# Optimization experiments

Hardware: AMD Instinct MI355X
Metric: run time of the kernel (lower is better)

The kernel has to match this reference:

```python
import jax, jax.numpy as jnp
import numpy as np

H, W = 64, 64
C = 256
NH = 8
WS = 8
SS = 4
N = WS * WS
HD = C // NH
HIDDEN = 4 * C
CPB_HIDDEN = 512
EPS = 1e-6


def _window_partition(x, ws):
    B, H_, W_, C_ = x.shape
    x = x.reshape(B, H_ // ws, ws, W_ // ws, ws, C_).transpose(0, 1, 3, 2, 4, 5)
    return x.reshape(-1, ws, ws, C_)


def _window_reverse(win, ws, H_, W_):
    B = win.shape[0] // ((H_ // ws) * (W_ // ws))
    x = win.reshape(B, H_ // ws, W_ // ws, ws, ws, -1).transpose(0, 1, 3, 2, 4, 5)
    return x.reshape(B, H_, W_, -1)


def _coords_table():
    # (1, 2*WS-1, 2*WS-1, 2) log-spaced continuous relative coords (SwinV2 CPB)
    ch = np.arange(-(WS - 1), WS)
    cw = np.arange(-(WS - 1), WS)
    t = np.stack(np.meshgrid(ch, cw, indexing='ij'), axis=-1)[None].astype(np.float32)
    t = t / (WS - 1) * 8.0
    t = np.sign(t) * np.log2(np.abs(t) + 1.0) / np.log2(8.0)
    return t.astype(np.float32)


def _rpe_index():
    coords = np.stack(np.meshgrid(np.arange(WS), np.arange(WS), indexing='ij'))
    cf = coords.reshape(2, -1)
    rel = (cf[:, :, None] - cf[:, None, :]).transpose(1, 2, 0)
    rel[:, :, 0] += WS - 1
    rel[:, :, 1] += WS - 1
    rel[:, :, 0] *= 2 * WS - 1
    return rel.sum(-1)  # (N, N) int


def _attn_mask():
    img = np.zeros((1, H, W, 1), np.float32)
    cnt = 0
    for hs in (slice(0, -WS), slice(-WS, -SS), slice(-SS, None)):
        for ws_ in (slice(0, -WS), slice(-WS, -SS), slice(-SS, None)):
            img[:, hs, ws_, :] = cnt
            cnt += 1
    mw = img.reshape(1, H // WS, WS, W // WS, WS, 1).transpose(0, 1, 3, 2, 4, 5).reshape(-1, N)
    am = mw[:, None, :] - mw[:, :, None]
    return np.where(am != 0, -100.0, 0.0).astype(np.float32)  # (nW, N, N)


_TABLE = jnp.asarray(_coords_table())
_RPE = jnp.asarray(_rpe_index().reshape(-1))
_AMASK = jnp.asarray(_attn_mask())


def setup_inputs() -> dict:
    key = jax.random.key(0)
    ks = jax.random.split(key, 12)
    s = 0.02
    return {
        'x': jax.random.normal(ks[0], (32, H * W, C), jnp.float32),
        'qkv_w': jax.random.normal(ks[1], (C, 3 * C), jnp.float32) * s,
        'q_bias': jnp.zeros((C,), jnp.float32),
        'v_bias': jnp.zeros((C,), jnp.float32),
        'logit_scale': jnp.log(10.0 * jnp.ones((NH, 1, 1), jnp.float32)),
        'cpb_w1': jax.random.normal(ks[2], (2, CPB_HIDDEN), jnp.float32) * s,
        'cpb_b1': jnp.zeros((CPB_HIDDEN,), jnp.float32),
        'cpb_w2': jax.random.normal(ks[3], (CPB_HIDDEN, NH), jnp.float32) * s,
        'proj_w': jax.random.normal(ks[4], (C, C), jnp.float32) * s,
        'proj_b': jnp.zeros((C,), jnp.float32),
        'norm1_scale': jnp.ones((C,), jnp.float32),
        'norm1_bias': jnp.zeros((C,), jnp.float32),
        'norm2_scale': jnp.ones((C,), jnp.float32),
        'norm2_bias': jnp.zeros((C,), jnp.float32),
        'fc1_w': jax.random.normal(ks[5], (C, HIDDEN), jnp.float32) * s,
        'fc1_b': jnp.zeros((HIDDEN,), jnp.float32),
        'fc2_w': jax.random.normal(ks[6], (HIDDEN, C), jnp.float32) * s,
        'fc2_b': jnp.zeros((C,), jnp.float32),
    }


def _layernorm(y, scale, bias):
    mu = jnp.mean(y, axis=-1, keepdims=True)
    var = jnp.mean(jnp.square(y - mu), axis=-1, keepdims=True)
    return (y - mu) * jax.lax.rsqrt(var + EPS) * scale + bias


def _l2n(t):
    return t * jax.lax.rsqrt(jnp.maximum(jnp.sum(t * t, axis=-1, keepdims=True), 1e-12))


def reference(x, qkv_w, q_bias, v_bias, logit_scale, cpb_w1, cpb_b1, cpb_w2,
              proj_w, proj_b, norm1_scale, norm1_bias, norm2_scale, norm2_bias,
              fc1_w, fc1_b, fc2_w, fc2_b):
    B, L, C_ = x.shape
    nW = _AMASK.shape[0]
    shortcut = x

    # cyclic shift + window partition
    xi = x.reshape(B, H, W, C_)
    xi = jnp.roll(xi, (-SS, -SS), axis=(1, 2))
    xw = _window_partition(xi, WS).reshape(-1, N, C_)  # (B_, N, C)
    B_ = xw.shape[0]

    # qkv with q/v bias only (k bias is zero)
    qkv_bias = jnp.concatenate([q_bias, jnp.zeros_like(v_bias), v_bias])
    qkv = xw @ qkv_w + qkv_bias
    qkv = qkv.reshape(B_, N, 3, NH, HD).transpose(2, 0, 3, 1, 4)
    q, k, v = qkv[0], qkv[1], qkv[2]  # (B_, NH, N, HD)

    # cosine attention with learned clamped logit scale
    attn = jnp.einsum('bhnd,bhmd->bhnm', _l2n(q), _l2n(k))
    scale = jnp.exp(jnp.minimum(logit_scale, np.log(100.0)))  # (NH,1,1)
    attn = attn * scale

    # continuous-position-bias MLP -> relative position bias, 16*sigmoid
    bias_table = jax.nn.relu(_TABLE @ cpb_w1 + cpb_b1) @ cpb_w2  # (1,2WS-1,2WS-1,NH)
    bias_table = bias_table.reshape(-1, NH)
    rpb = bias_table[_RPE].reshape(N, N, NH).transpose(2, 0, 1)  # (NH,N,N)
    attn = attn + (16.0 * jax.nn.sigmoid(rpb))[None]

    # shifted-window mask
    attn = attn.reshape(B_ // nW, nW, NH, N, N) + _AMASK[None, :, None]
    attn = jax.nn.softmax(attn.reshape(B_, NH, N, N), axis=-1)

    out = jnp.einsum('bhnm,bhmd->bnhd', attn, v).reshape(B_, N, C_)
    out = out @ proj_w + proj_b

    # window reverse + reverse cyclic shift
    out = _window_reverse(out.reshape(-1, WS, WS, C_), WS, H, W)
    out = jnp.roll(out, (SS, SS), axis=(1, 2)).reshape(B, L, C_)

    # SwinV2 post-norm residuals
    x1 = shortcut + _layernorm(out, norm1_scale, norm1_bias)
    h = jax.nn.gelu(x1 @ fc1_w + fc1_b) @ fc2_w + fc2_b
    return x1 + _layernorm(h, norm2_scale, norm2_bias)
```

## Files before the change

### kernel.cpp

```cpp
#include <hip/hip_runtime.h>

typedef __bf16 bf16;
typedef __bf16 bf16x8 __attribute__((ext_vector_type(8)));
typedef __bf16 bf16x4 __attribute__((ext_vector_type(4)));
typedef float  f32x4  __attribute__((ext_vector_type(4)));

#define MFMA16(a, b, c) __builtin_amdgcn_mfma_f32_16x16x32_bf16(a, b, c, 0, 0, 0)

__device__ __forceinline__ void gload_lds16(const void* g, void* l) {
    __builtin_amdgcn_global_load_lds((const __attribute__((address_space(1))) void*)g,
                                     (__attribute__((address_space(3))) void*)l, 16, 0, 0);
}

__device__ __forceinline__ long win2orig(long r) {
    long b = r >> 12; int rem = (int)(r & 4095);
    int widx = rem >> 6, t = rem & 63;
    int rp = ((widx >> 3) << 3) + (t >> 3), cp = ((widx & 7) << 3) + (t & 7);
    int rr = (rp + 4) & 63, cc = (cp + 4) & 63;
    return (b << 12) + rr * 64 + cc;
}

template <int GELU>
__global__ __launch_bounds__(256) void gemm_bt(const bf16* __restrict__ A,
                                               const bf16* __restrict__ Bt,
                                               const float* __restrict__ bias,
                                               bf16* __restrict__ C,
                                               int M, int N, int K) {
    __shared__ bf16 As[2][4096];
    __shared__ bf16 Bs[2][4096];
    const int t = threadIdx.x;
    const int w = t >> 6, l = t & 63;
    const int l15 = l & 15, q4 = l >> 4;
    const int wm = w >> 1, wn = w & 1;

    const unsigned gx = gridDim.x;
    const unsigned nwg = gx * gridDim.y;
    const unsigned id0 = blockIdx.y * gx + blockIdx.x;
    const unsigned swz = (id0 & 7u) * (nwg >> 3) + (id0 >> 3);
    const unsigned bx = swz % gx, by = swz / gx;

    const long row0 = (long)by * 128;
    const int col0 = (int)bx * 128;

    const bf16* aP = A + (row0 + w * 16 + l15) * (long)K + q4 * 8;
    const bf16* bP = Bt + (long)(col0 + w * 16 + l15) * K + q4 * 8;
    const long step64 = 64L * K;

    f32x4 acc[4][4];
#pragma unroll
    for (int i = 0; i < 4; i++)
#pragma unroll
        for (int j = 0; j < 4; j++)
#pragma unroll
            for (int r = 0; r < 4; r++) acc[i][j][r] = 0.f;

    const int KT = K >> 5;

    gload_lds16(aP,          &As[0][w * 512]);
    gload_lds16(aP + step64, &As[0][w * 512 + 2048]);
    gload_lds16(bP,          &Bs[0][w * 512]);
    gload_lds16(bP + step64, &Bs[0][w * 512 + 2048]);
    aP += 32; bP += 32;
    gload_lds16(aP,          &As[1][w * 512]);
    gload_lds16(aP + step64, &As[1][w * 512 + 2048]);
    gload_lds16(bP,          &Bs[1][w * 512]);
    gload_lds16(bP + step64, &Bs[1][w * 512 + 2048]);
    aP += 32; bP += 32;

    for (int kt = 0; kt < KT; ++kt) {
        const int cur = kt & 1;
        if (kt < KT - 1) { asm volatile("s_waitcnt vmcnt(4)" ::: "memory"); }
        else             { asm volatile("s_waitcnt vmcnt(0)" ::: "memory"); }
        __builtin_amdgcn_s_barrier();
        asm volatile("" ::: "memory");

        bf16x8 af[4], bfv[4];
#pragma unroll
        for (int mi = 0; mi < 4; mi++) af[mi] = *(const bf16x8*)(&As[cur][(wm * 4 + mi) * 512 + l * 8]);
#pragma unroll
        for (int nj = 0; nj < 4; nj++) bfv[nj] = *(const bf16x8*)(&Bs[cur][(wn * 4 + nj) * 512 + l * 8]);

        asm volatile("s_waitcnt lgkmcnt(0)" ::: "memory");
        __builtin_amdgcn_sched_barrier(0);
        __builtin_amdgcn_s_barrier();
        asm volatile("" ::: "memory");

        if (kt + 2 < KT) {
            gload_lds16(aP,          &As[cur][w * 512]);
            gload_lds16(aP + step64, &As[cur][w * 512 + 2048]);
            gload_lds16(bP,          &Bs[cur][w * 512]);
            gload_lds16(bP + step64, &Bs[cur][w * 512 + 2048]);
            aP += 32; bP += 32;
        }
        __builtin_amdgcn_sched_barrier(0);

#pragma unroll
        for (int mi = 0; mi < 4; mi++)
#pragma unroll
            for (int nj = 0; nj < 4; nj++) acc[mi][nj] = MFMA16(af[mi], bfv[nj], acc[mi][nj]);
    }

    float cb[4];
#pragma unroll
    for (int nj = 0; nj < 4; nj++) cb[nj] = bias[col0 + wn * 64 + nj * 16 + l15];

#pragma unroll
    for (int mi = 0; mi < 4; mi++) {
#pragma unroll
        for (int reg = 0; reg < 4; reg++) {
            long r = row0 + wm * 64 + mi * 16 + q4 * 4 + reg;
            bf16* cpn = C + r * (long)N + col0 + wn * 64 + l15;
#pragma unroll
            for (int nj = 0; nj < 4; nj++) {
                float v = acc[mi][nj][reg] + cb[nj];
                if (GELU) {
                    float v2 = v * v;
                    float tt = v * fmaf(v2, -0.10294702f, -2.30218094f);
                    float e = __builtin_amdgcn_exp2f(tt);
                    v = v * __builtin_amdgcn_rcpf(1.f + e);
                }
                cpn[nj * 16] = (bf16)v;
            }
        }
    }
}

__global__ __launch_bounds__(64) void attn_kernel(const bf16* __restrict__ qkv,
                                                  const float* __restrict__ bias16,
                                                  const float* __restrict__ logit_scale,
                                                  bf16* __restrict__ outp) {
    __shared__ bf16 P[64 * 72];
    __shared__ bf16 Vt[32 * 72];
    const int unit = blockIdx.x;
    const int w = unit >> 3, h = unit & 7;
    const int l = threadIdx.x;
    const int l15 = l & 15, q4 = l >> 4;
    const bf16* base = qkv + (long)w * 64 * 768;

    {
        const bf16* vp = base + l * 768 + 512 + h * 32;
#pragma unroll
        for (int c = 0; c < 4; c++) {
            bf16x8 vv = *(const bf16x8*)(vp + c * 8);
#pragma unroll
            for (int j = 0; j < 8; j++) Vt[(c * 8 + j) * 72 + l] = vv[j];
        }
    }

    const float scale = __expf(fminf(logit_scale[h], 4.605170186f));

    bf16x8 qf[4], kf[4];
#pragma unroll
    for (int mi = 0; mi < 4; mi++) {
        const bf16* p = base + (mi * 16 + l15) * 768 + h * 32 + q4 * 8;
        bf16x8 xv = *(const bf16x8*)p;
        float fv[8]; float ss = 0.f;
#pragma unroll
        for (int j = 0; j < 8; j++) { fv[j] = (float)xv[j]; ss += fv[j] * fv[j]; }
        ss += __shfl_xor(ss, 16); ss += __shfl_xor(ss, 32);
        float rs = rsqrtf(fmaxf(ss, 1e-12f));
#pragma unroll
        for (int j = 0; j < 8; j++) qf[mi][j] = (bf16)(fv[j] * rs);
    }
#pragma unroll
    for (int nj = 0; nj < 4; nj++) {
        const bf16* p = base + (nj * 16 + l15) * 768 + 256 + h * 32 + q4 * 8;
        bf16x8 xv = *(const bf16x8*)p;
        float fv[8]; float ss = 0.f;
#pragma unroll
        for (int j = 0; j < 8; j++) { fv[j] = (float)xv[j]; ss += fv[j] * fv[j]; }
        ss += __shfl_xor(ss, 16); ss += __shfl_xor(ss, 32);
        float rs = rsqrtf(fmaxf(ss, 1e-12f));
#pragma unroll
        for (int j = 0; j < 8; j++) kf[nj][j] = (bf16)(fv[j] * rs);
    }

    f32x4 acc[4][4];
#pragma unroll
    for (int i = 0; i < 4; i++)
#pragma unroll
        for (int j = 0; j < 4; j++)
#pragma unroll
            for (int r = 0; r < 4; r++) acc[i][j][r] = 0.f;
#pragma unroll
    for (int mi = 0; mi < 4; mi++)
#pragma unroll
        for (int nj = 0; nj < 4; nj++) acc[mi][nj] = MFMA16(qf[mi], kf[nj], acc[mi][nj]);

    const int widx = w & 63, wr = widx >> 3, wc = widx & 7;
    const bool edge = (wr == 7) || (wc == 7);
    int crid[4];
    if (edge) {
#pragma unroll
        for (int nj = 0; nj < 4; nj++) {
            int m = nj * 16 + l15;
            int R = wr * 8 + (m >> 3), Cc = wc * 8 + (m & 7);
            crid[nj] = ((R < 56) ? 0 : (R < 60 ? 1 : 2)) * 3 + ((Cc < 56) ? 0 : (Cc < 60 ? 1 : 2));
        }
    }
    const float* bh = bias16 + h * 4096;
#pragma unroll
    for (int mi = 0; mi < 4; mi++) {
#pragma unroll
        for (int reg = 0; reg < 4; reg++) {
            int n = mi * 16 + q4 * 4 + reg;
            const float* bp = bh + n * 64;
            int nrid = 0;
            if (edge) {
                int R = wr * 8 + (n >> 3), Cc = wc * 8 + (n & 7);
                nrid = ((R < 56) ? 0 : (R < 60 ? 1 : 2)) * 3 + ((Cc < 56) ? 0 : (Cc < 60 ? 1 : 2));
            }
#pragma unroll
            for (int nj = 0; nj < 4; nj++) {
                float v = acc[mi][nj][reg] * scale + bp[nj * 16 + l15];
                if (edge && nrid != crid[nj]) v -= 100.f;
                acc[mi][nj][reg] = v;
            }
        }
    }

#pragma unroll
    for (int mi = 0; mi < 4; mi++) {
#pragma unroll
        for (int reg = 0; reg < 4; reg++) {
            float mx = fmaxf(fmaxf(acc[mi][0][reg], acc[mi][1][reg]),
                             fmaxf(acc[mi][2][reg], acc[mi][3][reg]));
            mx = fmaxf(mx, __shfl_xor(mx, 1));
            mx = fmaxf(mx, __shfl_xor(mx, 2));
            mx = fmaxf(mx, __shfl_xor(mx, 4));
            mx = fmaxf(mx, __shfl_xor(mx, 8));
            float s = 0.f;
#pragma unroll
            for (int nj = 0; nj < 4; nj++) {
                float e = __expf(acc[mi][nj][reg] - mx);
                acc[mi][nj][reg] = e; s += e;
            }
            s += __shfl_xor(s, 1); s += __shfl_xor(s, 2);
            s += __shfl_xor(s, 4); s += __shfl_xor(s, 8);
            float inv = 1.f / s;
            int n = mi * 16 + q4 * 4 + reg;
#pragma unroll
            for (int nj = 0; nj < 4; nj++)
                P[n * 72 + nj * 16 + l15] = (bf16)(acc[mi][nj][reg] * inv);
        }
    }
    __syncthreads();

    f32x4 o[4][2];
#pragma unroll
    for (int i = 0; i < 4; i++)
#pragma unroll
        for (int j = 0; j < 2; j++)
#pragma unroll
            for (int r = 0; r < 4; r++) o[i][j][r] = 0.f;
#pragma unroll
    for (int ks = 0; ks < 2; ks++) {
        bf16x8 vf[2];
#pragma unroll
        for (int nj = 0; nj < 2; nj++) vf[nj] = *(const bf16x8*)(&Vt[(nj * 16 + l15) * 72 + ks * 32 + q4 * 8]);
#pragma unroll
        for (int mi = 0; mi < 4; mi++) {
            bf16x8 pf = *(const bf16x8*)(&P[(mi * 16 + l15) * 72 + ks * 32 + q4 * 8]);
#pragma unroll
            for (int nj = 0; nj < 2; nj++) o[mi][nj] = MFMA16(pf, vf[nj], o[mi][nj]);
        }
    }

    bf16* op = outp + (long)w * 64 * 256 + h * 32;
#pragma unroll
    for (int mi = 0; mi < 4; mi++)
#pragma unroll
        for (int reg = 0; reg < 4; reg++) {
            int tok = mi * 16 + q4 * 4 + reg;
#pragma unroll
            for (int nj = 0; nj < 2; nj++)
                op[tok * 256 + nj * 16 + l15] = (bf16)o[mi][nj][reg];
        }
}

__global__ __launch_bounds__(256) void norm1_kernel(const bf16* __restrict__ pin,
                                                    const float* __restrict__ x,
                                                    const float* __restrict__ g,
                                                    const float* __restrict__ bb,
                                                    bf16* __restrict__ x1h) {
    const int tid = threadIdx.x;
    const int wid = tid >> 6, l = tid & 63;
    const long rl = (long)blockIdx.x * 4 + wid;
    bf16x4 v4 = *(const bf16x4*)(pin + rl * 256 + l * 4);
    float v[4]; float s = 0.f, sq = 0.f;
#pragma unroll
    for (int c = 0; c < 4; c++) { v[c] = (float)v4[c]; s += v[c]; sq += v[c] * v[c]; }
#pragma unroll
    for (int off = 1; off < 64; off <<= 1) { s += __shfl_xor(s, off); sq += __shfl_xor(sq, off); }
    float mu = s * 0.00390625f;
    float var = sq * 0.00390625f - mu * mu;
    float rstd = rsqrtf(var + 1e-6f);
    long orig = win2orig(rl);
    float4 xv = *(const float4*)(x + orig * 256 + l * 4);
    float4 gv = *(const float4*)(g + l * 4);
    float4 bv = *(const float4*)(bb + l * 4);
    bf16x4 oh;
    oh[0] = (bf16)(xv.x + ((v[0] - mu) * rstd * gv.x + bv.x));
    oh[1] = (bf16)(xv.y + ((v[1] - mu) * rstd * gv.y + bv.y));
    oh[2] = (bf16)(xv.z + ((v[2] - mu) * rstd * gv.z + bv.z));
    oh[3] = (bf16)(xv.w + ((v[3] - mu) * rstd * gv.w + bv.w));
    *(bf16x4*)(x1h + orig * 256 + l * 4) = oh;
}

__global__ __launch_bounds__(256) void norm2_kernel(const bf16* __restrict__ hin,
                                                    const bf16* __restrict__ x1h,
                                                    const float* __restrict__ g,
                                                    const float* __restrict__ bb,
                                                    float* __restrict__ outp) {
    const int tid = threadIdx.x;
    const int wid = tid >> 6, l = tid & 63;
    const long rl = (long)blockIdx.x * 4 + wid;
    bf16x4 v4 = *(const bf16x4*)(hin + rl * 256 + l * 4);
    float v[4]; float s = 0.f, sq = 0.f;
#pragma unroll
    for (int c = 0; c < 4; c++) { v[c] = (float)v4[c]; s += v[c]; sq += v[c] * v[c]; }
#pragma unroll
    for (int off = 1; off < 64; off <<= 1) { s += __shfl_xor(s, off); sq += __shfl_xor(sq, off); }
    float mu = s * 0.00390625f;
    float var = sq * 0.00390625f - mu * mu;
    float rstd = rsqrtf(var + 1e-6f);
    bf16x4 xv4 = *(const bf16x4*)(x1h + rl * 256 + l * 4);
    float4 gv = *(const float4*)(g + l * 4);
    float4 bv = *(const float4*)(bb + l * 4);
    float4 ov;
    ov.x = (float)xv4[0] + ((v[0] - mu) * rstd * gv.x + bv.x);
    ov.y = (float)xv4[1] + ((v[1] - mu) * rstd * gv.y + bv.y);
    ov.z = (float)xv4[2] + ((v[2] - mu) * rstd * gv.z + bv.z);
    ov.w = (float)xv4[3] + ((v[3] - mu) * rstd * gv.w + bv.w);
    *(float4*)(outp + rl * 256 + l * 4) = ov;
}

__global__ __launch_bounds__(256) void gather_cast(const float* __restrict__ x,
                                                   bf16* __restrict__ out) {
    const int tid = threadIdx.x;
    const int wid = tid >> 6, l = tid & 63;
    const long rl = (long)blockIdx.x * 4 + wid;
    long orig = win2orig(rl);
    float4 v = *(const float4*)(x + orig * 256 + l * 4);
    bf16x4 o = {(bf16)v.x, (bf16)v.y, (bf16)v.z, (bf16)v.w};
    *(bf16x4*)(out + rl * 256 + l * 4) = o;
}

__global__ void transpose_cast(const float* __restrict__ in, bf16* __restrict__ out, int K, int N) {
    int id = blockIdx.x * 256 + threadIdx.x;
    if (id < K * N) {
        int n = id / K, k = id - n * K;
        out[id] = (bf16)in[k * N + n];
    }
}

__global__ void build_qkv_bias(const float* __restrict__ qb, const float* __restrict__ vb,
                               float* __restrict__ out) {
    int i = blockIdx.x * 256 + threadIdx.x;
    if (i < 768) out[i] = (i < 256) ? qb[i] : ((i < 512) ? 0.f : vb[i - 512]);
}

__device__ __forceinline__ float cpcoord(int d) {
    float v = (float)d * (8.0f / 7.0f);
    float r = log2f(fabsf(v) + 1.0f) * (1.0f / 3.0f);
    return v < 0.f ? -r : r;
}

__global__ void cpb1(const float* __restrict__ w1, const float* __restrict__ b1,
                     const float* __restrict__ w2, float* __restrict__ tbl) {
    int a = threadIdx.x;
    if (a >= 225) return;
    int i = a / 15, j = a - i * 15;
    float t0 = cpcoord(i - 7), t1 = cpcoord(j - 7);
    float acc[8];
#pragma unroll
    for (int o = 0; o < 8; o++) acc[o] = 0.f;
    for (int jj = 0; jj < 512; jj++) {
        float hv = fmaf(t0, w1[jj], fmaf(t1, w1[512 + jj], b1[jj]));
        hv = fmaxf(hv, 0.f);
#pragma unroll
        for (int o = 0; o < 8; o++) acc[o] = fmaf(hv, w2[jj * 8 + o], acc[o]);
    }
#pragma unroll
    for (int o = 0; o < 8; o++) tbl[a * 8 + o] = acc[o];
}

__global__ void cpb2(const float* __restrict__ tbl, float* __restrict__ bias16) {
    int id = blockIdx.x * 256 + threadIdx.x;
    if (id >= 32768) return;
    int h = id >> 12, n = (id >> 6) & 63, m = id & 63;
    int r0 = (n >> 3) - (m >> 3) + 7;
    int r1 = (n & 7) - (m & 7) + 7;
    float v = tbl[(r0 * 15 + r1) * 8 + h];
    bias16[id] = 16.f / (1.f + __expf(-v));
}

extern "C" void kernel_launch(void* const* d_in, const int* in_sizes, int n_in,
                              void* d_out, int out_size, void* d_ws, size_t ws_size,
                              hipStream_t stream) {
    const float* x   = (const float*)d_in[0];
    const float* qkvw= (const float*)d_in[1];
    const float* qb  = (const float*)d_in[2];
    const float* vb  = (const float*)d_in[3];
    const float* ls  = (const float*)d_in[4];
    const float* cw1 = (const float*)d_in[5];
    const float* cb1 = (const float*)d_in[6];
    const float* cw2 = (const float*)d_in[7];
    const float* pw  = (const float*)d_in[8];
    const float* pb  = (const float*)d_in[9];
    const float* n1s = (const float*)d_in[10];
    const float* n1b = (const float*)d_in[11];
    const float* n2s = (const float*)d_in[12];
    const float* n2b = (const float*)d_in[13];
    const float* f1w = (const float*)d_in[14];
    const float* f1b = (const float*)d_in[15];
    const float* f2w = (const float*)d_in[16];
    const float* f2b = (const float*)d_in[17];

    char* ws = (char*)d_ws;
    if (ws_size < 471859200UL) return;
    bf16*  qkvBt   = (bf16*)(ws + 0);
    bf16*  projBt  = (bf16*)(ws + 393216);
    bf16*  fc1Bt   = (bf16*)(ws + 524288);
    bf16*  fc2Bt   = (bf16*)(ws + 1048576);
    float* qkvBias = (float*)(ws + 1572864);
    float* cpbTbl  = (float*)(ws + 1575936);
    float* bias16  = (float*)(ws + 1583360);
    bf16* xbf     = (bf16*)(ws + 2097152);
    bf16* qkvBuf  = (bf16*)(ws + 69206016);
    bf16* attnOut = (bf16*)(ws + 270532608);
    bf16* projOut = (bf16*)(ws + 337641472);
    bf16* x1h     = (bf16*)(ws + 404750336);
    bf16* hBuf    = (bf16*)(ws + 2097152);
    bf16* fc2Out  = (bf16*)(ws + 337641472);

    transpose_cast<<<768, 256, 0, stream>>>(qkvw, qkvBt, 256, 768);
    transpose_cast<<<256, 256, 0, stream>>>(pw, projBt, 256, 256);
    transpose_cast<<<1024, 256, 0, stream>>>(f1w, fc1Bt, 256, 1024);
    transpose_cast<<<1024, 256, 0, stream>>>(f2w, fc2Bt, 1024, 256);
    build_qkv_bias<<<3, 256, 0, stream>>>(qb, vb, qkvBias);
    cpb1<<<1, 256, 0, stream>>>(cw1, cb1, cw2, cpbTbl);
    cpb2<<<128, 256, 0, stream>>>(cpbTbl, bias16);

    gather_cast<<<32768, 256, 0, stream>>>(x, xbf);
    gemm_bt<0><<<dim3(6, 1024), 256, 0, stream>>>(xbf, qkvBt, qkvBias, qkvBuf, 131072, 768, 256);
    attn_kernel<<<16384, 64, 0, stream>>>(qkvBuf, bias16, ls, attnOut);
    gemm_bt<0><<<dim3(2, 1024), 256, 0, stream>>>(attnOut, projBt, pb, projOut, 131072, 256, 256);
    norm1_kernel<<<32768, 256, 0, stream>>>(projOut, x, n1s, n1b, x1h);
    gemm_bt<1><<<dim3(8, 1024), 256, 0, stream>>>(x1h, fc1Bt, f1b, hBuf, 131072, 1024, 256);
    gemm_bt<0><<<dim3(2, 1024), 256, 0, stream>>>(hBuf, fc2Bt, f2b, fc2Out, 131072, 256, 1024);
    norm2_kernel<<<32768, 256, 0, stream>>>(fc2Out, x1h, n2s, n2b, (float*)d_out);
}
```

Measured before the change: 1.030 ms.

## Enlarge GEMM tiles to 256x256 with 512 threads and K-step 64

The shared GEMM kernel moves from 128x128 tiles with 4 waves to 256x256 tiles with 8 waves, each wave computing 128x64. Each K iteration now covers 64 elements, split into two 32-wide halves with separate LDS reads, and all four GEMM launches get matching grids. The goal is more reuse of each loaded tile and fewer global loads and barriers per FLOP. The cost is 128KB of LDS per block and a larger accumulator array, which may lower occupancy. The fixed LDS layout with 256x256 tiles also assumes the 16-row staging per wave lines up with the fragment reads.

```diff
diff --git a/kernel.cpp b/kernel.cpp
--- a/kernel.cpp
+++ b/kernel.cpp
@@ -21,17 +21,17 @@
 }
 
 template <int GELU>
-__global__ __launch_bounds__(256) void gemm_bt(const bf16* __restrict__ A,
-                                               const bf16* __restrict__ Bt,
-                                               const float* __restrict__ bias,
-                                               bf16* __restrict__ C,
-                                               int M, int N, int K) {
-    __shared__ bf16 As[2][4096];
-    __shared__ bf16 Bs[2][4096];
+__global__ __launch_bounds__(512, 2) void gemm_bt(const bf16* __restrict__ A,
+                                                  const bf16* __restrict__ Bt,
+                                                  const float* __restrict__ bias,
+                                                  bf16* __restrict__ C,
+                                                  int M, int N, int K) {
+    __shared__ bf16 As[2][16384];
+    __shared__ bf16 Bs[2][16384];
     const int t = threadIdx.x;
     const int w = t >> 6, l = t & 63;
     const int l15 = l & 15, q4 = l >> 4;
-    const int wm = w >> 1, wn = w & 1;
+    const int wm = w >> 2, wn = w & 3;
 
     const unsigned gx = gridDim.x;
     const unsigned nwg = gx * gridDim.y;
@@ -39,76 +39,98 @@
     const unsigned swz = (id0 & 7u) * (nwg >> 3) + (id0 >> 3);
     const unsigned bx = swz % gx, by = swz / gx;
 
-    const long row0 = (long)by * 128;
-    const int col0 = (int)bx * 128;
-
-    const bf16* aP = A + (row0 + w * 16 + l15) * (long)K + q4 * 8;
-    const bf16* bP = Bt + (long)(col0 + w * 16 + l15) * K + q4 * 8;
-    const long step64 = 64L * K;
-
-    f32x4 acc[4][4];
-#pragma unroll
-    for (int i = 0; i < 4; i++)
+    const long row0 = (long)by * 256;
+    const int col0 = (int)bx * 256;
+
+    const bf16* aSrc0; const bf16* aSrc1; const bf16* aSrc2; const bf16* aSrc3;
+    const bf16* bSrc0; const bf16* bSrc1; const bf16* bSrc2; const bf16* bSrc3;
+    {
+        const long ar = row0 + (w * 2) * 16 + l15;
+        const long br = (long)col0 + (w * 2) * 16 + l15;
+        aSrc0 = A + ar * (long)K + q4 * 8;
+        aSrc1 = A + ar * (long)K + 32 + q4 * 8;
+        aSrc2 = A + (ar + 16) * (long)K + q4 * 8;
+        aSrc3 = A + (ar + 16) * (long)K + 32 + q4 * 8;
+        bSrc0 = Bt + br * (long)K + q4 * 8;
+        bSrc1 = Bt + br * (long)K + 32 + q4 * 8;
+        bSrc2 = Bt + (br + 16) * (long)K + q4 * 8;
+        bSrc3 = Bt + (br + 16) * (long)K + 32 + q4 * 8;
+    }
+
+#define STAGE(buf)                                         \
+    do {                                                   \
+        gload_lds16(aSrc0, &As[buf][w * 2048 + 0 * 512]);  \
+        gload_lds16(aSrc1, &As[buf][w * 2048 + 1 * 512]);  \
+        gload_lds16(aSrc2, &As[buf][w * 2048 + 2 * 512]);  \
+        gload_lds16(aSrc3, &As[buf][w * 2048 + 3 * 512]);  \
+        gload_lds16(bSrc0, &Bs[buf][w * 2048 + 0 * 512]);  \
+        gload_lds16(bSrc1, &Bs[buf][w * 2048 + 1 * 512]);  \
+        gload_lds16(bSrc2, &Bs[buf][w * 2048 + 2 * 512]);  \
+        gload_lds16(bSrc3, &Bs[buf][w * 2048 + 3 * 512]);  \
+        aSrc0 += 64; aSrc1 += 64; aSrc2 += 64; aSrc3 += 64;\
+        bSrc0 += 64; bSrc1 += 64; bSrc2 += 64; bSrc3 += 64;\
+    } while (0)
+
+    f32x4 acc[8][4];
+#pragma unroll
+    for (int i = 0; i < 8; i++)
 #pragma unroll
         for (int j = 0; j < 4; j++)
 #pragma unroll
             for (int r = 0; r < 4; r++) acc[i][j][r] = 0.f;
 
-    const int KT = K >> 5;
-
-    gload_lds16(aP,          &As[0][w * 512]);
-    gload_lds16(aP + step64, &As[0][w * 512 + 2048]);
-    gload_lds16(bP,          &Bs[0][w * 512]);
-    gload_lds16(bP + step64, &Bs[0][w * 512 + 2048]);
-    aP += 32; bP += 32;
-    gload_lds16(aP,          &As[1][w * 512]);
-    gload_lds16(aP + step64, &As[1][w * 512 + 2048]);
-    gload_lds16(bP,          &Bs[1][w * 512]);
-    gload_lds16(bP + step64, &Bs[1][w * 512 + 2048]);
-    aP += 32; bP += 32;
+    const int KT = K >> 6;
+
+    STAGE(0);
+    STAGE(1);
 
     for (int kt = 0; kt < KT; ++kt) {
         const int cur = kt & 1;
-        if (kt < KT - 1) { asm volatile("s_waitcnt vmcnt(4)" ::: "memory"); }
+        if (kt < KT - 1) { asm volatile("s_waitcnt vmcnt(8)" ::: "memory"); }
         else             { asm volatile("s_waitcnt vmcnt(0)" ::: "memory"); }
         __builtin_amdgcn_s_barrier();
         asm volatile("" ::: "memory");
 
-        bf16x8 af[4], bfv[4];
-#pragma unroll
-        for (int mi = 0; mi < 4; mi++) af[mi] = *(const bf16x8*)(&As[cur][(wm * 4 + mi) * 512 + l * 8]);
-#pragma unroll
-        for (int nj = 0; nj < 4; nj++) bfv[nj] = *(const bf16x8*)(&Bs[cur][(wn * 4 + nj) * 512 + l * 8]);
-
+        bf16x8 af[8], bfv[4];
+#pragma unroll
+        for (int mi = 0; mi < 8; mi++) af[mi] = *(const bf16x8*)(&As[cur][(wm * 8 + mi) * 1024 + l * 8]);
+#pragma unroll
+        for (int nj = 0; nj < 4; nj++) bfv[nj] = *(const bf16x8*)(&Bs[cur][(wn * 4 + nj) * 1024 + l * 8]);
+        asm volatile("s_waitcnt lgkmcnt(0)" ::: "memory");
+        __builtin_amdgcn_sched_barrier(0);
+#pragma unroll
+        for (int mi = 0; mi < 8; mi++)
+#pragma unroll
+            for (int nj = 0; nj < 4; nj++) acc[mi][nj] = MFMA16(af[mi], bfv[nj], acc[mi][nj]);
+
+#pragma unroll
+        for (int mi = 0; mi < 8; mi++) af[mi] = *(const bf16x8*)(&As[cur][(wm * 8 + mi) * 1024 + 512 + l * 8]);
+#pragma unroll
+        for (int nj = 0; nj < 4; nj++) bfv[nj] = *(const bf16x8*)(&Bs[cur][(wn * 4 + nj) * 1024 + 512 + l * 8]);
         asm volatile("s_waitcnt lgkmcnt(0)" ::: "memory");
         __builtin_amdgcn_sched_barrier(0);
         __builtin_amdgcn_s_barrier();
         asm volatile("" ::: "memory");
 
-        if (kt + 2 < KT) {
-            gload_lds16(aP,          &As[cur][w * 512]);
-            gload_lds16(aP + step64, &As[cur][w * 512 + 2048]);
-            gload_lds16(bP,          &Bs[cur][w * 512]);
-            gload_lds16(bP + step64, &Bs[cur][w * 512 + 2048]);
-            aP += 32; bP += 32;
-        }
+        if (kt + 2 < KT) STAGE(cur);
         __builtin_amdgcn_sched_barrier(0);
 
 #pragma unroll
-        for (int mi = 0; mi < 4; mi++)
+        for (int mi = 0; mi < 8; mi++)
 #pragma unroll
             for (int nj = 0; nj < 4; nj++) acc[mi][nj] = MFMA16(af[mi], bfv[nj], acc[mi][nj]);
     }
+#undef STAGE
 
     float cb[4];
 #pragma unroll
     for (int nj = 0; nj < 4; nj++) cb[nj] = bias[col0 + wn * 64 + nj * 16 + l15];
 
 #pragma unroll
-    for (int mi = 0; mi < 4; mi++) {
+    for (int mi = 0; mi < 8; mi++) {
 #pragma unroll
         for (int reg = 0; reg < 4; reg++) {
-            long r = row0 + wm * 64 + mi * 16 + q4 * 4 + reg;
+            long r = row0 + wm * 128 + mi * 16 + q4 * 4 + reg;
             bf16* cpn = C + r * (long)N + col0 + wn * 64 + l15;
 #pragma unroll
             for (int nj = 0; nj < 4; nj++) {
@@ -443,11 +465,11 @@
     cpb2<<<128, 256, 0, stream>>>(cpbTbl, bias16);
 
     gather_cast<<<32768, 256, 0, stream>>>(x, xbf);
-    gemm_bt<0><<<dim3(6, 1024), 256, 0, stream>>>(xbf, qkvBt, qkvBias, qkvBuf, 131072, 768, 256);
+    gemm_bt<0><<<dim3(3, 512), 512, 0, stream>>>(xbf, qkvBt, qkvBias, qkvBuf, 131072, 768, 256);
     attn_kernel<<<16384, 64, 0, stream>>>(qkvBuf, bias16, ls, attnOut);
-    gemm_bt<0><<<dim3(2, 1024), 256, 0, stream>>>(attnOut, projBt, pb, projOut, 131072, 256, 256);
+    gemm_bt<0><<<dim3(1, 512), 512, 0, stream>>>(attnOut, projBt, pb, projOut, 131072, 256, 256);
     norm1_kernel<<<32768, 256, 0, stream>>>(projOut, x, n1s, n1b, x1h);
-    gemm_bt<1><<<dim3(8, 1024), 256, 0, stream>>>(x1h, fc1Bt, f1b, hBuf, 131072, 1024, 256);
-    gemm_bt<0><<<dim3(2, 1024), 256, 0, stream>>>(hBuf, fc2Bt, f2b, fc2Out, 131072, 256, 1024);
+    gemm_bt<1><<<dim3(4, 512), 512, 0, stream>>>(x1h, fc1Bt, f1b, hBuf, 131072, 1024, 256);
+    gemm_bt<0><<<dim3(1, 512), 512, 0, stream>>>(hBuf, fc2Bt, f2b, fc2Out, 131072, 256, 1024);
     norm2_kernel<<<32768, 256, 0, stream>>>(fc2Out, x1h, n2s, n2b, (float*)d_out);
 }
```

After: 933.4 us. -9.4%, faster.
